# Kernel optimization log

Measured on AMD Instinct MI355X. Metric: run time of the kernel, lower is better.

The kernel has to match this reference:

```python
import jax, jax.numpy as jnp
import numpy as np

B, L, D_MODEL = 2, 2048, 1024
HEADS, DH, K = 8, 128, 64  # d_head = d_model // heads, kernel_width window
DILATIONS = np.array([1, 1, 2, 2, 4, 4, 8, 8], dtype=np.int32)  # per-head dilation


def setup_inputs() -> dict:
    key = jax.random.key(0)
    ks = jax.random.split(key, 8)
    s_in = 1.0 / np.sqrt(D_MODEL)       # kaiming-uniform-ish fan_in bound
    s_c = 1.0 / np.sqrt(HEADS * DH)
    return {
        "query": jax.random.normal(ks[0], (B, L, D_MODEL), dtype=jnp.float32),
        "key": jax.random.normal(ks[1], (B, L, D_MODEL), dtype=jnp.float32),
        "value": jax.random.normal(ks[2], (B, L, D_MODEL), dtype=jnp.float32),
        "Wq": jax.random.uniform(ks[3], (HEADS, DH, D_MODEL), minval=-s_in, maxval=s_in),
        "bq": jnp.zeros((HEADS, DH), dtype=jnp.float32),
        "Wk": jax.random.uniform(ks[4], (HEADS, DH, D_MODEL), minval=-s_in, maxval=s_in),
        "bk": jnp.zeros((HEADS, DH), dtype=jnp.float32),
        "Wv": jax.random.uniform(ks[5], (HEADS, DH, D_MODEL), minval=-s_in, maxval=s_in),
        "bv": jnp.zeros((HEADS, DH), dtype=jnp.float32),
        "Wc": jax.random.uniform(ks[6], (D_MODEL, HEADS * DH), minval=-s_c, maxval=s_c),
        "bc": jnp.zeros((D_MODEL,), dtype=jnp.float32),
    }


def reference(query, key, value, Wq, bq, Wk, bk, Wv, bv, Wc, bc):
    Lq = query.shape[-2]
    # per-head linear projections: [B,L,D] x [H,DH,D] -> [B,H,L,DH]
    q = jnp.einsum('bld,hed->bhle', query, Wq) + bq[:, None, :]
    k = jnp.einsum('bld,hed->bhle', key, Wk) + bk[:, None, :]
    v = jnp.einsum('bld,hed->bhle', value, Wv) + bv[:, None, :]

    # dilated, centered local windows (per-head dilation)
    offsets = jnp.arange(K) - (K - 1) // 2                     # [K]
    dil = jnp.asarray(DILATIONS)                               # [H]
    idx = (jnp.arange(Lq)[None, :, None]
           + offsets[None, None, :] * dil[:, None, None])      # [H, L, K]
    valid = (idx >= 0) & (idx < Lq)
    idxc = jnp.clip(idx, 0, Lq - 1)

    # gather per-head windows: x [B,H,L,DH], idx [H,L,K] -> [B,H,L,K,DH]
    gather = jax.vmap(lambda xh, ih: xh[:, ih], in_axes=(1, 0), out_axes=1)
    k_win = gather(k, idxc)
    v_win = gather(v, idxc)

    # banded attention (original applies no 1/sqrt(d) scaling)
    scores = jnp.einsum('bhld,bhlkd->bhlk', q, k_win)
    scores = jnp.where(valid[None], scores, jnp.asarray(-1e9, scores.dtype))
    attn = jax.nn.softmax(scores, axis=-1)
    out = jnp.einsum('bhlk,bhlkd->bhld', attn, v_win)

    # merge heads and collapse back to d_model
    out = out.transpose(0, 2, 1, 3).reshape(out.shape[0], Lq, HEADS * DH)
    return out @ Wc.T + bc
```

## Files before the change

### kernel.cpp

```cpp
#include <hip/hip_runtime.h>
#include <hip/hip_bf16.h>
#include <stdint.h>

#define NB 2
#define LQ 2048
#define DMODEL 1024
#define NH 8
#define DH 128
#define KWIN 64

typedef __attribute__((ext_vector_type(8))) short short8;
typedef __attribute__((ext_vector_type(4))) float f32x4;

__device__ __forceinline__ ushort f2bf(float f) {
  uint u = __float_as_uint(f);
  return (ushort)((u + 0x7fffu + ((u >> 16) & 1u)) >> 16);
}
__device__ __forceinline__ float bflo(uint u) { return __uint_as_float(u << 16); }
__device__ __forceinline__ float bfhi(uint u) { return __uint_as_float(u & 0xffff0000u); }

__global__ void cvt_qkv(const float4* __restrict__ a, const float4* __restrict__ b,
                        const float4* __restrict__ c, ushort* __restrict__ da,
                        ushort* __restrict__ db, ushort* __restrict__ dc, int n4) {
  int stride = gridDim.x * blockDim.x;
  for (int i = blockIdx.x * blockDim.x + threadIdx.x; i < n4; i += stride) {
    float4 x = a[i], y = b[i], z = c[i];
    *(ushort4*)(da + 4 * (size_t)i) = make_ushort4(f2bf(x.x), f2bf(x.y), f2bf(x.z), f2bf(x.w));
    *(ushort4*)(db + 4 * (size_t)i) = make_ushort4(f2bf(y.x), f2bf(y.y), f2bf(y.z), f2bf(y.w));
    *(ushort4*)(dc + 4 * (size_t)i) = make_ushort4(f2bf(z.x), f2bf(z.y), f2bf(z.z), f2bf(z.w));
  }
}

__global__ void cvt_w(const float4* __restrict__ a, const float4* __restrict__ b,
                      const float4* __restrict__ c, const float4* __restrict__ d,
                      ushort* __restrict__ da, ushort* __restrict__ db,
                      ushort* __restrict__ dc, ushort* __restrict__ dd, int n4) {
  int stride = gridDim.x * blockDim.x;
  for (int i = blockIdx.x * blockDim.x + threadIdx.x; i < n4; i += stride) {
    float4 x = a[i], y = b[i], z = c[i], w = d[i];
    *(ushort4*)(da + 4 * (size_t)i) = make_ushort4(f2bf(x.x), f2bf(x.y), f2bf(x.z), f2bf(x.w));
    *(ushort4*)(db + 4 * (size_t)i) = make_ushort4(f2bf(y.x), f2bf(y.y), f2bf(y.z), f2bf(y.w));
    *(ushort4*)(dc + 4 * (size_t)i) = make_ushort4(f2bf(z.x), f2bf(z.y), f2bf(z.z), f2bf(z.w));
    *(ushort4*)(dd + 4 * (size_t)i) = make_ushort4(f2bf(w.x), f2bf(w.y), f2bf(w.z), f2bf(w.w));
  }
}

template <int OUT_BF16>
__global__ __launch_bounds__(256, 2) void gemm_bt(
    const ushort* __restrict__ A0, const ushort* __restrict__ B0,
    const float* __restrict__ c0, void* __restrict__ D0,
    const ushort* __restrict__ A1, const ushort* __restrict__ B1,
    const float* __restrict__ c1, void* __restrict__ D1,
    const ushort* __restrict__ A2, const ushort* __restrict__ B2,
    const float* __restrict__ c2, void* __restrict__ D2,
    int M, int N, int Kd) {
  const int z = blockIdx.z;
  const ushort* A = (z == 0) ? A0 : ((z == 1) ? A1 : A2);
  const ushort* Bt = (z == 0) ? B0 : ((z == 1) ? B1 : B2);
  const float* bias = (z == 0) ? c0 : ((z == 1) ? c1 : c2);
  void* Cv = (z == 0) ? D0 : ((z == 1) ? D1 : D2);

  __shared__ ushort As[128 * 32];
  __shared__ ushort Bs[128 * 32];

  const int tid = threadIdx.x;
  const int wave = tid >> 6, lane = tid & 63;
  const int wm = wave >> 1, wn = wave & 1;
  const int lrow = lane & 15, kgrp = lane >> 4;

  const int m0 = blockIdx.y * 128, n0 = blockIdx.x * 128;

  const int b0 = tid * 16;
  const int b1 = b0 + 4096;
  const int r0 = b0 >> 6, cc0 = (b0 & 63) >> 1;
  const int r1 = b1 >> 6, cc1 = (b1 & 63) >> 1;

  f32x4 acc[4][4] = {};

  for (int kt = 0; kt < Kd; kt += 32) {
    __builtin_amdgcn_global_load_lds(
        (const __attribute__((address_space(1))) void*)(A + (size_t)(m0 + r0) * Kd + kt + cc0),
        (__attribute__((address_space(3))) void*)(As + (b0 >> 1)), 16, 0, 0);
    __builtin_amdgcn_global_load_lds(
        (const __attribute__((address_space(1))) void*)(A + (size_t)(m0 + r1) * Kd + kt + cc1),
        (__attribute__((address_space(3))) void*)(As + (b1 >> 1)), 16, 0, 0);
    __builtin_amdgcn_global_load_lds(
        (const __attribute__((address_space(1))) void*)(Bt + (size_t)(n0 + r0) * Kd + kt + cc0),
        (__attribute__((address_space(3))) void*)(Bs + (b0 >> 1)), 16, 0, 0);
    __builtin_amdgcn_global_load_lds(
        (const __attribute__((address_space(1))) void*)(Bt + (size_t)(n0 + r1) * Kd + kt + cc1),
        (__attribute__((address_space(3))) void*)(Bs + (b1 >> 1)), 16, 0, 0);
    __syncthreads();

    short8 af[4], bfr[4];
#pragma unroll
    for (int m = 0; m < 4; ++m)
      af[m] = *(const short8*)(As + (wm * 64 + m * 16 + lrow) * 32 + kgrp * 8);
#pragma unroll
    for (int n = 0; n < 4; ++n)
      bfr[n] = *(const short8*)(Bs + (wn * 64 + n * 16 + lrow) * 32 + kgrp * 8);
#pragma unroll
    for (int m = 0; m < 4; ++m)
#pragma unroll
      for (int n = 0; n < 4; ++n)
        acc[m][n] = __builtin_amdgcn_mfma_f32_16x16x32_bf16(af[m], bfr[n], acc[m][n], 0, 0, 0);
    __syncthreads();
  }

  const int cbase = n0 + wn * 64;
  const int rbase = m0 + wm * 64;
  float bv[4];
#pragma unroll
  for (int n = 0; n < 4; ++n) bv[n] = bias[cbase + n * 16 + lrow];

#pragma unroll
  for (int m = 0; m < 4; ++m) {
#pragma unroll
    for (int n = 0; n < 4; ++n) {
      const int col = cbase + n * 16 + lrow;
#pragma unroll
      for (int j = 0; j < 4; ++j) {
        const int row = rbase + m * 16 + kgrp * 4 + j;
        float val = acc[m][n][j] + bv[n];
        if (OUT_BF16) {
          ((ushort*)Cv)[(size_t)row * N + col] = f2bf(val);
        } else {
          ((float*)Cv)[(size_t)row * N + col] = val;
        }
      }
    }
  }
}

__global__ __launch_bounds__(128) void banded_attn_mfma(
    const ushort* __restrict__ qp, const ushort* __restrict__ kp,
    const ushort* __restrict__ vp, ushort* __restrict__ ao) {
  __shared__ ushort Qs[32 * 128];
  __shared__ ushort Ks[96 * 128];
  __shared__ ushort Vs[112 * 128];
  __shared__ ushort Ps[2][16 * 104];
  __shared__ ushort Os[2][16 * 128];

  const int tid = threadIdx.x;
  const int wv = tid >> 6;
  const int lane = tid & 63;
  const int lrow = lane & 15, kgrp = lane >> 4;

  const int blk = blockIdx.x;
  const int chunk = blk & 63;
  const int h = (blk >> 6) & 7;
  const int b = blk >> 9;
  const int sh = h >> 1;
  const int dil = 1 << sh;
  const int Ld = LQ >> sh;
  const int rres = chunk >> (6 - sh);
  const int tile = chunk & ((64 >> sh) - 1);
  const int t0 = tile << 5;
  const int p0 = t0 - 32;

  const size_t headoff = (size_t)h * DH;
  const size_t bbase = (size_t)b * LQ * (NH * DH);

  const int srow = lane >> 4;
  const int sc = lane & 15;
  for (int it = wv; it < 60; it += 2) {
    int rbase, pstart;
    const ushort* g;
    ushort* ld;
    if (it < 8) {
      rbase = it * 4; pstart = t0; g = qp; ld = Qs;
    } else if (it < 32) {
      rbase = (it - 8) * 4; pstart = p0; g = kp; ld = Ks;
    } else {
      rbase = (it - 32) * 4; pstart = p0; g = vp; ld = Vs;
    }
    int row = rbase + srow;
    int key = (row ^ (row >> 3)) & 7;
    int cs = sc ^ key;
    int t = pstart + row;
    t = t < 0 ? 0 : (t >= Ld ? Ld - 1 : t);
    int l = rres + t * dil;
    const ushort* src = g + bbase + (size_t)l * (NH * DH) + headoff + cs * 8;
    __builtin_amdgcn_global_load_lds(
        (const __attribute__((address_space(1))) void*)src,
        (__attribute__((address_space(3))) void*)(ld + rbase * 128), 16, 0, 0);
  }
  __syncthreads();

  const int iblk = wv << 4;
  f32x4 accs[5] = {};
#pragma unroll
  for (int ks = 0; ks < 4; ++ks) {
    const int qrow = iblk + lrow;
    const int qslot = (ks * 4 + kgrp) ^ ((qrow ^ (qrow >> 3)) & 7);
    short8 qf = *(const short8*)(Qs + qrow * 128 + qslot * 8);
#pragma unroll
    for (int t = 0; t < 5; ++t) {
      const int krow = (wv + t) * 16 + lrow;
      const int kslot = (ks * 4 + kgrp) ^ ((krow ^ (krow >> 3)) & 7);
      short8 kf = *(const short8*)(Ks + krow * 128 + kslot * 8);
      accs[t] = __builtin_amdgcn_mfma_f32_16x16x32_bf16(qf, kf, accs[t], 0, 0, 0);
    }
  }

  float dens[4];
#pragma unroll
  for (int j = 0; j < 4; ++j) {
    const int i_b = iblk + kgrp * 4 + j;
    float mj = -1e30f;
#pragma unroll
    for (int t = 0; t < 5; ++t) {
      const int jj = (wv + t) * 16 + lrow;
      const int p = p0 + jj;
      const bool ok = (jj >= i_b + 1) && (jj <= i_b + 64) && (p >= 0) && (p < Ld);
      float v = ok ? accs[t][j] : -1e30f;
      accs[t][j] = v;
      mj = fmaxf(mj, v);
    }
#pragma unroll
    for (int off = 1; off < 16; off <<= 1) mj = fmaxf(mj, __shfl_xor(mj, off));
    float dj = 0.f;
#pragma unroll
    for (int t = 0; t < 5; ++t) {
      float e = __expf(accs[t][j] - mj);
      accs[t][j] = e;
      dj += e;
    }
#pragma unroll
    for (int off = 1; off < 16; off <<= 1) dj += __shfl_xor(dj, off);
    dens[j] = dj;
  }

  ushort* Pw = Ps[wv];
#pragma unroll
  for (int j = 0; j < 4; ++j) {
    const int prow = kgrp * 4 + j;
#pragma unroll
    for (int t = 0; t < 5; ++t) Pw[prow * 104 + t * 16 + lrow] = f2bf(accs[t][j]);
    Pw[prow * 104 + 80 + lrow] = 0;
  }

  f32x4 accv[8] = {};
#pragma unroll
  for (int ks = 0; ks < 3; ++ks) {
    short8 pf = *(const short8*)(Pw + lrow * 104 + ks * 32 + kgrp * 8);
#pragma unroll
    for (int dt = 0; dt < 8; ++dt) {
      short8 vf;
#pragma unroll
      for (int rr = 0; rr < 8; ++rr) {
        const int vrow = iblk + ks * 32 + kgrp * 8 + rr;
        const int d = dt * 16 + lrow;
        const int slot = (d >> 3) ^ ((vrow ^ (vrow >> 3)) & 7);
        vf[rr] = (short)Vs[vrow * 128 + slot * 8 + (d & 7)];
      }
      accv[dt] = __builtin_amdgcn_mfma_f32_16x16x32_bf16(pf, vf, accv[dt], 0, 0, 0);
    }
  }

  ushort* Ow = Os[wv];
#pragma unroll
  for (int j = 0; j < 4; ++j) {
    const float inv = 1.f / dens[j];
    const int orow = kgrp * 4 + j;
#pragma unroll
    for (int dt = 0; dt < 8; ++dt)
      Ow[orow * 128 + dt * 16 + lrow] = f2bf(accv[dt][j] * inv);
  }
#pragma unroll
  for (int pass = 0; pass < 4; ++pass) {
    const int i_loc = pass * 4 + srow;
    const int tq = t0 + iblk + i_loc;
    const int l = rres + tq * dil;
    short8 vvv = *(const short8*)(Ow + i_loc * 128 + sc * 8);
    *(short8*)(ao + bbase + (size_t)l * (NH * DH) + headoff + sc * 8) = vvv;
  }
}

extern "C" void kernel_launch(void* const* d_in, const int* in_sizes, int n_in,
                              void* d_out, int out_size, void* d_ws, size_t ws_size,
                              hipStream_t stream) {
  const float* q = (const float*)d_in[0];
  const float* k = (const float*)d_in[1];
  const float* v = (const float*)d_in[2];
  const float* Wq = (const float*)d_in[3];
  const float* bq = (const float*)d_in[4];
  const float* Wk = (const float*)d_in[5];
  const float* bk = (const float*)d_in[6];
  const float* Wv = (const float*)d_in[7];
  const float* bv = (const float*)d_in[8];
  const float* Wc = (const float*)d_in[9];
  const float* bc = (const float*)d_in[10];

  const size_t NIN = (size_t)NB * LQ * DMODEL;
  const size_t NW = (size_t)NH * DH * DMODEL;

  ushort* qin = (ushort*)d_ws;
  ushort* kin = qin + NIN;
  ushort* vin = kin + NIN;
  ushort* wqb = vin + NIN;
  ushort* wkb = wqb + NW;
  ushort* wvb = wkb + NW;
  ushort* wcb = wvb + NW;
  ushort* qp = wcb + NW;
  ushort* kp = qp + NIN;
  ushort* vp = kp + NIN;
  ushort* aob = vp + NIN;

  hipLaunchKernelGGL(cvt_qkv, dim3(2048), dim3(256), 0, stream,
                     (const float4*)q, (const float4*)k, (const float4*)v,
                     qin, kin, vin, (int)(NIN / 4));
  hipLaunchKernelGGL(cvt_w, dim3(1024), dim3(256), 0, stream,
                     (const float4*)Wq, (const float4*)Wk, (const float4*)Wv, (const float4*)Wc,
                     wqb, wkb, wvb, wcb, (int)(NW / 4));

  dim3 g1(DMODEL / 128, (NB * LQ) / 128, 3);
  hipLaunchKernelGGL((gemm_bt<1>), g1, dim3(256), 0, stream,
                     qin, wqb, bq, (void*)qp,
                     kin, wkb, bk, (void*)kp,
                     vin, wvb, bv, (void*)vp,
                     NB * LQ, DMODEL, DMODEL);

  hipLaunchKernelGGL(banded_attn_mfma, dim3(NB * NH * 64), dim3(128), 0, stream,
                     qp, kp, vp, aob);

  dim3 g2(DMODEL / 128, (NB * LQ) / 128, 1);
  hipLaunchKernelGGL((gemm_bt<0>), g2, dim3(256), 0, stream,
                     aob, wcb, bc, d_out,
                     aob, wcb, bc, d_out,
                     aob, wcb, bc, d_out,
                     NB * LQ, DMODEL, DMODEL);
}
```

Baseline: 106.9 us.

## Double-buffer GEMM LDS tiles, swizzle block order, raise occupancy bound

```diff
diff --git a/kernel.cpp b/kernel.cpp
--- a/kernel.cpp
+++ b/kernel.cpp
@@ -46,7 +46,7 @@
 }
 
 template <int OUT_BF16>
-__global__ __launch_bounds__(256, 2) void gemm_bt(
+__global__ __launch_bounds__(256, 4) void gemm_bt(
     const ushort* __restrict__ A0, const ushort* __restrict__ B0,
     const float* __restrict__ c0, void* __restrict__ D0,
     const ushort* __restrict__ A1, const ushort* __restrict__ B1,
@@ -54,58 +54,82 @@
     const ushort* __restrict__ A2, const ushort* __restrict__ B2,
     const float* __restrict__ c2, void* __restrict__ D2,
     int M, int N, int Kd) {
-  const int z = blockIdx.z;
+  const int gx = gridDim.x, gy = gridDim.y;
+  const int nblk = gx * gy * gridDim.z;
+  const int fid = (blockIdx.z * gy + blockIdx.y) * gx + blockIdx.x;
+  const int cpx = nblk >> 3;
+  const int nid = (fid & 7) * cpx + (fid >> 3);
+  const int z = nid / (gx * gy);
+  const int rem = nid % (gx * gy);
+  const int m0 = (rem / gx) * 128;
+  const int n0 = (rem % gx) * 128;
+
   const ushort* A = (z == 0) ? A0 : ((z == 1) ? A1 : A2);
   const ushort* Bt = (z == 0) ? B0 : ((z == 1) ? B1 : B2);
   const float* bias = (z == 0) ? c0 : ((z == 1) ? c1 : c2);
   void* Cv = (z == 0) ? D0 : ((z == 1) ? D1 : D2);
 
-  __shared__ ushort As[128 * 32];
-  __shared__ ushort Bs[128 * 32];
+  __shared__ ushort As[2][128 * 32];
+  __shared__ ushort Bs[2][128 * 32];
 
   const int tid = threadIdx.x;
   const int wave = tid >> 6, lane = tid & 63;
   const int wm = wave >> 1, wn = wave & 1;
   const int lrow = lane & 15, kgrp = lane >> 4;
 
-  const int m0 = blockIdx.y * 128, n0 = blockIdx.x * 128;
-
   const int b0 = tid * 16;
   const int b1 = b0 + 4096;
   const int r0 = b0 >> 6, cc0 = (b0 & 63) >> 1;
   const int r1 = b1 >> 6, cc1 = (b1 & 63) >> 1;
 
+  const ushort* gA0 = A + (size_t)(m0 + r0) * Kd + cc0;
+  const ushort* gA1 = A + (size_t)(m0 + r1) * Kd + cc1;
+  const ushort* gB0 = Bt + (size_t)(n0 + r0) * Kd + cc0;
+  const ushort* gB1 = Bt + (size_t)(n0 + r1) * Kd + cc1;
+
+  auto stage = [&](int buf, int kt) {
+    __builtin_amdgcn_global_load_lds(
+        (const __attribute__((address_space(1))) void*)(gA0 + kt),
+        (__attribute__((address_space(3))) void*)(As[buf] + (b0 >> 1)), 16, 0, 0);
+    __builtin_amdgcn_global_load_lds(
+        (const __attribute__((address_space(1))) void*)(gA1 + kt),
+        (__attribute__((address_space(3))) void*)(As[buf] + (b1 >> 1)), 16, 0, 0);
+    __builtin_amdgcn_global_load_lds(
+        (const __attribute__((address_space(1))) void*)(gB0 + kt),
+        (__attribute__((address_space(3))) void*)(Bs[buf] + (b0 >> 1)), 16, 0, 0);
+    __builtin_amdgcn_global_load_lds(
+        (const __attribute__((address_space(1))) void*)(gB1 + kt),
+        (__attribute__((address_space(3))) void*)(Bs[buf] + (b1 >> 1)), 16, 0, 0);
+  };
+
   f32x4 acc[4][4] = {};
 
-  for (int kt = 0; kt < Kd; kt += 32) {
-    __builtin_amdgcn_global_load_lds(
-        (const __attribute__((address_space(1))) void*)(A + (size_t)(m0 + r0) * Kd + kt + cc0),
-        (__attribute__((address_space(3))) void*)(As + (b0 >> 1)), 16, 0, 0);
-    __builtin_amdgcn_global_load_lds(
-        (const __attribute__((address_space(1))) void*)(A + (size_t)(m0 + r1) * Kd + kt + cc1),
-        (__attribute__((address_space(3))) void*)(As + (b1 >> 1)), 16, 0, 0);
-    __builtin_amdgcn_global_load_lds(
-        (const __attribute__((address_space(1))) void*)(Bt + (size_t)(n0 + r0) * Kd + kt + cc0),
-        (__attribute__((address_space(3))) void*)(Bs + (b0 >> 1)), 16, 0, 0);
-    __builtin_amdgcn_global_load_lds(
-        (const __attribute__((address_space(1))) void*)(Bt + (size_t)(n0 + r1) * Kd + kt + cc1),
-        (__attribute__((address_space(3))) void*)(Bs + (b1 >> 1)), 16, 0, 0);
-    __syncthreads();
-
+  auto compute = [&](int buf) {
     short8 af[4], bfr[4];
 #pragma unroll
     for (int m = 0; m < 4; ++m)
-      af[m] = *(const short8*)(As + (wm * 64 + m * 16 + lrow) * 32 + kgrp * 8);
+      af[m] = *(const short8*)(As[buf] + (wm * 64 + m * 16 + lrow) * 32 + kgrp * 8);
 #pragma unroll
     for (int n = 0; n < 4; ++n)
-      bfr[n] = *(const short8*)(Bs + (wn * 64 + n * 16 + lrow) * 32 + kgrp * 8);
+      bfr[n] = *(const short8*)(Bs[buf] + (wn * 64 + n * 16 + lrow) * 32 + kgrp * 8);
 #pragma unroll
     for (int m = 0; m < 4; ++m)
 #pragma unroll
       for (int n = 0; n < 4; ++n)
         acc[m][n] = __builtin_amdgcn_mfma_f32_16x16x32_bf16(af[m], bfr[n], acc[m][n], 0, 0, 0);
+  };
+
+  const int nt = Kd >> 5;
+  stage(0, 0);
+  __syncthreads();
+  int cur = 0;
+  for (int it = 0; it < nt - 1; ++it) {
+    stage(cur ^ 1, (it + 1) << 5);
+    compute(cur);
     __syncthreads();
-  }
+    cur ^= 1;
+  }
+  compute(cur);
 
   const int cbase = n0 + wn * 64;
   const int rbase = m0 + wm * 64;
```

Result: faster. 101.1 us (-5.5%).
